# Performance work log

Measured on AMD Instinct MI355X. Metric: run time of the kernel, lower is better.

Reference implementation:

```python
import jax, jax.numpy as jnp
import numpy as np

D_MODEL = 1024
D_STATE = 16
BATCH = 2
SEQ = 2048


def setup_inputs() -> dict:
    key = jax.random.key(0)
    k1, k2, k3, k4, k5 = jax.random.split(key, 5)
    x = jax.random.normal(k1, (BATCH, SEQ, D_MODEL), dtype=jnp.float32)
    log_A_diag = jax.random.normal(k2, (D_MODEL, D_STATE), dtype=jnp.float32)
    B_w = jax.random.normal(k3, (D_STATE, D_MODEL), dtype=jnp.float32) / np.sqrt(D_MODEL)
    C_w = jax.random.normal(k4, (D_MODEL, D_STATE), dtype=jnp.float32) / np.sqrt(D_STATE)
    D_vec = jax.random.normal(k5, (D_MODEL,), dtype=jnp.float32)
    return {"x": x, "log_A_diag": log_A_diag, "B_w": B_w, "C_w": C_w, "D_vec": D_vec}


def reference(x, log_A_diag, B_w, C_w, D_vec):
    # x: (B, L, D)
    B, L, D = x.shape
    pad = 2 * L
    A_bar = jnp.exp(-jnp.exp(log_A_diag))          # (D, S), in (0, 1)
    B_t = jnp.einsum('bld,sd->bls', x, B_w)        # B projection: (B, L, S)
    k_idx = jnp.arange(L, dtype=x.dtype)
    kernel = A_bar[..., None] ** k_idx             # (D, S, L) exponential kernel
    # zero-padded FFT convolution along time axis
    kernel_fft = jnp.fft.rfft(kernel, n=pad, axis=-1)                 # (D, S, L+1)
    B_fft = jnp.fft.rfft(B_t.transpose(0, 2, 1), n=pad, axis=-1)      # (B, S, L+1)
    conv_fft = kernel_fft[None] * B_fft[:, None]                      # (B, D, S, L+1)
    conv = jnp.fft.irfft(conv_fft, n=pad, axis=-1)[..., :L]           # (B, D, S, L)
    # C projection fused over state dim; equivalent to permute->einsum('blds,ds->bld')
    y = jnp.einsum('bdsl,ds->bld', conv, C_w)
    y = y + D_vec[None, None, :] * x               # skip connection
    return y  # dropout is identity in eval mode
```

## Files before the change

### kernel.cpp

```cpp
#include <hip/hip_runtime.h>

#define D_MODEL 1024
#define D_STATE 16
#define BATCH   2
#define SEQ     2048
#define CHUNK   32
#define NCHUNK  (SEQ / CHUNK)

__global__ __launch_bounds__(256) void k_bt(const float* __restrict__ x,
                                            const float* __restrict__ Bw,
                                            float* __restrict__ bt) {
    const int t    = threadIdx.x;
    const int wave = t >> 6;
    const int lane = t & 63;

    float4 bw[4][4];
    const float* bwp = Bw + (wave * 4) * D_MODEL + lane * 16;
#pragma unroll
    for (int i = 0; i < 4; ++i)
#pragma unroll
        for (int k = 0; k < 4; ++k)
            bw[i][k] = *(const float4*)(bwp + i * D_MODEL + k * 4);

    const int ROWS = (BATCH * SEQ) / gridDim.x;
    const int row0 = blockIdx.x * ROWS;
    for (int r = 0; r < ROWS; ++r) {
        const int row = row0 + r;
        const float* xr = x + (size_t)row * D_MODEL + lane * 16;
        float4 xv[4];
#pragma unroll
        for (int k = 0; k < 4; ++k) xv[k] = *(const float4*)(xr + k * 4);

        float acc[4] = {0.f, 0.f, 0.f, 0.f};
#pragma unroll
        for (int i = 0; i < 4; ++i) {
#pragma unroll
            for (int k = 0; k < 4; ++k) {
                acc[i] += xv[k].x * bw[i][k].x;
                acc[i] += xv[k].y * bw[i][k].y;
                acc[i] += xv[k].z * bw[i][k].z;
                acc[i] += xv[k].w * bw[i][k].w;
            }
        }
#pragma unroll
        for (int m = 1; m < 64; m <<= 1) {
#pragma unroll
            for (int i = 0; i < 4; ++i) acc[i] += __shfl_xor(acc[i], m, 64);
        }
        if (lane == 0)
            *(float4*)(bt + (size_t)row * D_STATE + wave * 4) =
                make_float4(acc[0], acc[1], acc[2], acc[3]);
    }
}

__global__ __launch_bounds__(256) void k_locals(const float* __restrict__ bt,
                                                const float* __restrict__ logA,
                                                float* __restrict__ f) {
    const int blk = blockIdx.x;
    const int dt  = blk & 63;
    const int c   = (blk >> 6) & 63;
    const int b   = blk >> 12;

    __shared__ float sbt[CHUNK * D_STATE];
    const int t = threadIdx.x;
    if (t < (CHUNK * D_STATE) / 4)
        ((float4*)sbt)[t] =
            ((const float4*)(bt + ((size_t)b * SEQ + c * CHUNK) * D_STATE))[t];
    __syncthreads();

    const int s  = t & 15;
    const int dd = t >> 4;
    const int d  = dt * 16 + dd;
    const float A = expf(-expf(logA[d * D_STATE + s]));
    float h = 0.f;
#pragma unroll
    for (int j = 0; j < CHUNK; ++j) h = A * h + sbt[j * D_STATE + s];
    f[(((size_t)b * NCHUNK + c) * D_MODEL + d) * D_STATE + s] = h;
}

__global__ __launch_bounds__(256) void k_carry(const float* __restrict__ logA,
                                               float* __restrict__ f) {
    const int t = blockIdx.x * 256 + threadIdx.x;
    const int s = t & 15;
    const int d = (t >> 4) & (D_MODEL - 1);
    const int b = t >> 14;
    const float A = expf(-expf(logA[d * D_STATE + s]));
    float AT = A;
#pragma unroll
    for (int i = 0; i < 5; ++i) AT *= AT;

    float carry = 0.f;
    const size_t stride = (size_t)D_MODEL * D_STATE;
    size_t idx = (size_t)b * NCHUNK * stride + (size_t)d * D_STATE + s;
    for (int c = 0; c < NCHUNK; ++c) {
        const float fl = f[idx];
        f[idx] = carry;
        carry = AT * carry + fl;
        idx += stride;
    }
}

__global__ __launch_bounds__(256) void k_final(const float* __restrict__ x,
                                               const float* __restrict__ logA,
                                               const float* __restrict__ Cw,
                                               const float* __restrict__ Dv,
                                               const float* __restrict__ bt,
                                               const float* __restrict__ carry,
                                               float* __restrict__ y) {
    const int blk = blockIdx.x;
    const int dt  = blk & 3;
    const int c   = (blk >> 2) & 63;
    const int b   = blk >> 8;
    const int t   = threadIdx.x;
    const int d   = dt * 256 + t;

    __shared__ float sbt[CHUNK * D_STATE];
    if (t < (CHUNK * D_STATE) / 4)
        ((float4*)sbt)[t] =
            ((const float4*)(bt + ((size_t)b * SEQ + c * CHUNK) * D_STATE))[t];
    __syncthreads();

    float A[D_STATE], C[D_STATE], h[D_STATE];
    const float* lp = logA + (size_t)d * D_STATE;
    const float* cp = Cw + (size_t)d * D_STATE;
    const float* hp = carry + (((size_t)b * NCHUNK + c) * D_MODEL + d) * D_STATE;
#pragma unroll
    for (int s = 0; s < D_STATE; ++s) {
        A[s] = expf(-expf(lp[s]));
        C[s] = cp[s];
        h[s] = hp[s];
    }
    const float dv = Dv[d];

    const size_t rowbase = ((size_t)b * SEQ + c * CHUNK) * D_MODEL + d;
    const float* xp = x + rowbase;
    float*       yp = y + rowbase;

#pragma unroll 4
    for (int j = 0; j < CHUNK; ++j) {
        float acc = dv * xp[(size_t)j * D_MODEL];
#pragma unroll
        for (int s = 0; s < D_STATE; ++s) {
            h[s] = A[s] * h[s] + sbt[j * D_STATE + s];
            acc += C[s] * h[s];
        }
        yp[(size_t)j * D_MODEL] = acc;
    }
}

extern "C" void kernel_launch(void* const* d_in, const int* in_sizes, int n_in,
                              void* d_out, int out_size, void* d_ws, size_t ws_size,
                              hipStream_t stream) {
    const float* x    = (const float*)d_in[0];
    const float* logA = (const float*)d_in[1];
    const float* Bw   = (const float*)d_in[2];
    const float* Cw   = (const float*)d_in[3];
    const float* Dv   = (const float*)d_in[4];
    float* y = (float*)d_out;

    float* bt = (float*)d_ws;
    float* f  = bt + (size_t)BATCH * SEQ * D_STATE;

    hipLaunchKernelGGL(k_bt,     dim3(512),  dim3(256), 0, stream, x, Bw, bt);
    hipLaunchKernelGGL(k_locals, dim3(BATCH * NCHUNK * (D_MODEL / 16)),  dim3(256), 0, stream, bt, logA, f);
    hipLaunchKernelGGL(k_carry,  dim3((BATCH * D_MODEL * D_STATE) / 256), dim3(256), 0, stream, logA, f);
    hipLaunchKernelGGL(k_final,  dim3(BATCH * NCHUNK * (D_MODEL / 256)),  dim3(256), 0, stream, x, logA, Cw, Dv, bt, f, y);
}
```

Measured before the change: 104.5 us.

## Replace chunk-local plus carry kernels with a single sequential scan over grouped inputs

Merges the per-chunk local scan and the carry propagation into one kernel. Each (batch, d, s) thread walks the whole sequence, consuming four timesteps per step from a new interleaved float4 layout written by the projection kernel, and uses the A^4 stride factorization. The final kernel now reads B projections straight from global memory instead of staging them in shared memory. This removes one launch and the intermediate f round-trip, at the cost of a long 2048-step serial dependency per thread and only 32K threads in the scan.

```diff
diff --git a/kernel.cpp b/kernel.cpp
--- a/kernel.cpp
+++ b/kernel.cpp
@@ -6,10 +6,12 @@
 #define SEQ     2048
 #define CHUNK   32
 #define NCHUNK  (SEQ / CHUNK)
+#define NGRP    (SEQ / 4)
 
 __global__ __launch_bounds__(256) void k_bt(const float* __restrict__ x,
                                             const float* __restrict__ Bw,
-                                            float* __restrict__ bt) {
+                                            float* __restrict__ bt,
+                                            float* __restrict__ btg) {
     const int t    = threadIdx.x;
     const int wave = t >> 6;
     const int lane = t & 63;
@@ -47,56 +49,42 @@
 #pragma unroll
             for (int i = 0; i < 4; ++i) acc[i] += __shfl_xor(acc[i], m, 64);
         }
-        if (lane == 0)
+        if (lane == 0) {
             *(float4*)(bt + (size_t)row * D_STATE + wave * 4) =
                 make_float4(acc[0], acc[1], acc[2], acc[3]);
+            const int b = row >> 11;
+            const int l = row & (SEQ - 1);
+            float* p = btg + (((size_t)(b * NGRP + (l >> 2)) * D_STATE + wave * 4) << 2) + (l & 3);
+#pragma unroll
+            for (int i = 0; i < 4; ++i) p[i * 4] = acc[i];
+        }
     }
 }
 
-__global__ __launch_bounds__(256) void k_locals(const float* __restrict__ bt,
-                                                const float* __restrict__ logA,
-                                                float* __restrict__ f) {
-    const int blk = blockIdx.x;
-    const int dt  = blk & 63;
-    const int c   = (blk >> 6) & 63;
-    const int b   = blk >> 12;
+__global__ __launch_bounds__(128) void k_scan(const float* __restrict__ btg,
+                                              const float* __restrict__ logA,
+                                              float* __restrict__ carry) {
+    const int g = blockIdx.x * 128 + threadIdx.x;
+    const int s = g & 15;
+    const int d = (g >> 4) & (D_MODEL - 1);
+    const int b = g >> 14;
 
-    __shared__ float sbt[CHUNK * D_STATE];
-    const int t = threadIdx.x;
-    if (t < (CHUNK * D_STATE) / 4)
-        ((float4*)sbt)[t] =
-            ((const float4*)(bt + ((size_t)b * SEQ + c * CHUNK) * D_STATE))[t];
-    __syncthreads();
+    const float A  = expf(-expf(logA[d * D_STATE + s]));
+    const float A2 = A * A;
+    const float A4 = A2 * A2;
 
-    const int s  = t & 15;
-    const int dd = t >> 4;
-    const int d  = dt * 16 + dd;
-    const float A = expf(-expf(logA[d * D_STATE + s]));
+    const float4* bp = (const float4*)btg + (size_t)b * NGRP * D_STATE + s;
+    size_t ci = (size_t)b * NCHUNK * (D_MODEL * D_STATE) + d * D_STATE + s;
+
     float h = 0.f;
+    for (int c = 0; c < NCHUNK; ++c) {
+        carry[ci] = h;
+        ci += D_MODEL * D_STATE;
 #pragma unroll
-    for (int j = 0; j < CHUNK; ++j) h = A * h + sbt[j * D_STATE + s];
-    f[(((size_t)b * NCHUNK + c) * D_MODEL + d) * D_STATE + s] = h;
-}
-
-__global__ __launch_bounds__(256) void k_carry(const float* __restrict__ logA,
-                                               float* __restrict__ f) {
-    const int t = blockIdx.x * 256 + threadIdx.x;
-    const int s = t & 15;
-    const int d = (t >> 4) & (D_MODEL - 1);
-    const int b = t >> 14;
-    const float A = expf(-expf(logA[d * D_STATE + s]));
-    float AT = A;
-#pragma unroll
-    for (int i = 0; i < 5; ++i) AT *= AT;
-
-    float carry = 0.f;
-    const size_t stride = (size_t)D_MODEL * D_STATE;
-    size_t idx = (size_t)b * NCHUNK * stride + (size_t)d * D_STATE + s;
-    for (int c = 0; c < NCHUNK; ++c) {
-        const float fl = f[idx];
-        f[idx] = carry;
-        carry = AT * carry + fl;
-        idx += stride;
+        for (int gg = 0; gg < CHUNK / 4; ++gg) {
+            const float4 v = bp[(size_t)(c * (CHUNK / 4) + gg) * D_STATE];
+            h = h * A4 + (((v.x * A + v.y) * A + v.z) * A + v.w);
+        }
     }
 }
 
@@ -109,21 +97,15 @@
                                                float* __restrict__ y) {
     const int blk = blockIdx.x;
     const int dt  = blk & 3;
-    const int c   = (blk >> 2) & 63;
+    const int c   = (blk >> 2) & (NCHUNK - 1);
     const int b   = blk >> 8;
     const int t   = threadIdx.x;
     const int d   = dt * 256 + t;
 
-    __shared__ float sbt[CHUNK * D_STATE];
-    if (t < (CHUNK * D_STATE) / 4)
-        ((float4*)sbt)[t] =
-            ((const float4*)(bt + ((size_t)b * SEQ + c * CHUNK) * D_STATE))[t];
-    __syncthreads();
-
     float A[D_STATE], C[D_STATE], h[D_STATE];
     const float* lp = logA + (size_t)d * D_STATE;
     const float* cp = Cw + (size_t)d * D_STATE;
-    const float* hp = carry + (((size_t)b * NCHUNK + c) * D_MODEL + d) * D_STATE;
+    const float* hp = carry + ((size_t)(b * NCHUNK + c) * D_MODEL + d) * D_STATE;
 #pragma unroll
     for (int s = 0; s < D_STATE; ++s) {
         A[s] = expf(-expf(lp[s]));
@@ -132,7 +114,8 @@
     }
     const float dv = Dv[d];
 
-    const size_t rowbase = ((size_t)b * SEQ + c * CHUNK) * D_MODEL + d;
+    const float* btrow = bt + (size_t)(b * SEQ + c * CHUNK) * D_STATE;
+    const size_t rowbase = (size_t)(b * SEQ + c * CHUNK) * D_MODEL + d;
     const float* xp = x + rowbase;
     float*       yp = y + rowbase;
 
@@ -141,7 +124,7 @@
         float acc = dv * xp[(size_t)j * D_MODEL];
 #pragma unroll
         for (int s = 0; s < D_STATE; ++s) {
-            h[s] = A[s] * h[s] + sbt[j * D_STATE + s];
+            h[s] = A[s] * h[s] + btrow[j * D_STATE + s];
             acc += C[s] * h[s];
         }
         yp[(size_t)j * D_MODEL] = acc;
@@ -158,11 +141,11 @@
     const float* Dv   = (const float*)d_in[4];
     float* y = (float*)d_out;
 
-    float* bt = (float*)d_ws;
-    float* f  = bt + (size_t)BATCH * SEQ * D_STATE;
+    float* bt    = (float*)d_ws;
+    float* btg   = bt  + (size_t)BATCH * SEQ * D_STATE;
+    float* carry = btg + (size_t)BATCH * SEQ * D_STATE;
 
-    hipLaunchKernelGGL(k_bt,     dim3(512),  dim3(256), 0, stream, x, Bw, bt);
-    hipLaunchKernelGGL(k_locals, dim3(BATCH * NCHUNK * (D_MODEL / 16)),  dim3(256), 0, stream, bt, logA, f);
-    hipLaunchKernelGGL(k_carry,  dim3((BATCH * D_MODEL * D_STATE) / 256), dim3(256), 0, stream, logA, f);
-    hipLaunchKernelGGL(k_final,  dim3(BATCH * NCHUNK * (D_MODEL / 256)),  dim3(256), 0, stream, x, logA, Cw, Dv, bt, f, y);
+    hipLaunchKernelGGL(k_bt,    dim3(512), dim3(256), 0, stream, x, Bw, bt, btg);
+    hipLaunchKernelGGL(k_scan,  dim3((BATCH * D_MODEL * D_STATE) / 128), dim3(128), 0, stream, btg, logA, carry);
+    hipLaunchKernelGGL(k_final, dim3(BATCH * NCHUNK * (D_MODEL / 256)),  dim3(256), 0, stream, x, logA, Cw, Dv, bt, carry, y);
 }
```

Result: slower. 116.8 us (+11.8%).
